# Optimization experiments

Hardware: AMD Instinct MI355X
Metric: run time of the kernel (lower is better)

Reference implementation:

```python
import jax, jax.numpy as jnp
import numpy as np

B, C, H, W = 2, 8, 256, 512


def _k3(x):
    """e_prod_KernelChannels3: 3x3 unroll -> [B,C,9,H,W].
    Channel k holds the neighbour at offset (k//3-1, k%3-1); middle (k=4) is ones
    ('e of middle = 1' per the docstring). ce arg of the torch module is unused."""
    b, c, h, w = x.shape
    p = jnp.pad(x, ((0, 0), (0, 0), (1, 1), (1, 1)))
    s = lambda dy, dx: p[:, :, dy:dy + h, dx:dx + w]
    return jnp.stack([s(0, 0), s(0, 1), s(0, 2),
                      s(1, 0), jnp.ones_like(x), s(1, 2),
                      s(2, 0), s(2, 1), s(2, 2)], axis=2)


def _forward(e, ce):
    b, c, h, w = e.shape
    e3 = _k3(e)    # kernel3(e, ce)
    ce3 = _k3(ce)  # kernel3(ce, e)
    e3p = jnp.pad(e3, ((0, 0), (0, 0), (0, 0), (1, 1), (1, 1)))
    ce3p = jnp.pad(ce3, ((0, 0), (0, 0), (0, 0), (1, 1), (1, 1)))
    E = lambda k: e3[:, :, k]
    Cc = lambda k: ce3[:, :, k]
    # torch pad-slices: ':-2'->start 0, '1:-1'->start 1, '2:'->start 2
    Ep = lambda k, r, cc: e3p[:, :, k, r:r + h, cc:cc + w]
    Cp = lambda k, r, cc: ce3p[:, :, k, r:r + h, cc:cc + w]

    def sel(ecands, ccands):
        es = jnp.stack(ecands, 0)          # [K,B,C,H,W]
        idx = jnp.argmax(jnp.stack(ccands, 0), axis=0)
        return jnp.take_along_axis(es, idx[None], axis=0)[0]

    e00 = E(0) * Ep(0, 0, 0)
    e04 = E(2) * Ep(2, 0, 2)
    e40 = E(6) * Ep(6, 2, 0)
    e44 = E(8) * Ep(8, 2, 2)
    e10 = sel([E(0) * Ep(3, 0, 0), E(3) * Ep(0, 1, 0)],
              [Cc(0) * Cp(3, 0, 0), Cc(3) * Cp(0, 1, 0)])
    e20 = sel([E(0) * Ep(6, 0, 0), E(3) * Ep(3, 1, 0), E(6) * Ep(0, 2, 0)],
              [Cc(0) * Cp(6, 0, 0), Cc(3) * Cp(3, 1, 0), Cc(6) * Cp(0, 2, 0)])
    e30 = sel([E(3) * Ep(6, 1, 0), E(6) * Ep(3, 2, 0)],
              [Cc(3) * Cp(6, 1, 0), Cc(6) * Cp(3, 2, 0)])
    e14 = sel([E(2) * Ep(5, 0, 2), E(5) * Ep(2, 1, 2)],
              [Cc(2) * Cp(5, 0, 2), Cc(5) * Cp(2, 1, 2)])
    # NOTE: source uses ce3_pad channel 3 (not 5) in the middle candidate -- kept faithfully
    e24 = sel([E(2) * Ep(8, 0, 2), E(5) * Ep(5, 1, 2), E(8) * Ep(2, 2, 2)],
              [Cc(2) * Cp(8, 0, 2), Cc(5) * Cp(3, 1, 2), Cc(8) * Cp(2, 2, 2)])
    e34 = sel([E(5) * Ep(8, 1, 2), E(8) * Ep(5, 2, 2)],
              [Cc(5) * Cp(8, 1, 2), Cc(8) * Cp(5, 2, 2)])
    e01 = sel([E(0) * Ep(1, 0, 0), E(1) * Ep(0, 0, 1)],
              [Cc(0) * Cp(1, 0, 0), Cc(1) * Cp(0, 0, 1)])
    e02 = sel([E(0) * Ep(2, 0, 0), E(1) * Ep(1, 0, 1), E(2) * Ep(0, 0, 2)],
              [Cc(0) * Cp(2, 0, 0), Cc(1) * Cp(1, 0, 1), Cc(2) * Cp(0, 0, 2)])
    e03 = sel([E(1) * Ep(2, 0, 1), E(2) * Ep(1, 0, 2)],
              [Cc(1) * Cp(2, 0, 1), Cc(2) * Cp(1, 0, 2)])
    e41 = sel([E(6) * Ep(7, 2, 0), E(7) * Ep(6, 2, 1)],
              [Cc(6) * Cp(7, 2, 0), Cc(7) * Cp(6, 2, 1)])
    e42 = sel([E(6) * Ep(8, 2, 0), E(7) * Ep(7, 2, 1), E(8) * Ep(6, 2, 2)],
              [Cc(6) * Cp(8, 2, 0), Cc(7) * Cp(7, 2, 1), Cc(8) * Cp(6, 2, 2)])
    e43 = sel([E(7) * Ep(8, 2, 1), E(8) * Ep(7, 2, 2)],
              [Cc(7) * Cp(8, 2, 1), Cc(8) * Cp(7, 2, 2)])
    return jnp.stack([e00, e01, e02, e03, e04,
                      e10, E(0), E(1), E(2), e14,
                      e20, E(3), E(4), E(5), e24,
                      e30, E(6), E(7), E(8), e34,
                      e40, e41, e42, e43, e44], axis=2)  # [B,C,25,H,W]


def setup_inputs() -> dict:
    key = jax.random.key(0)
    k1, k2 = jax.random.split(key)
    e = jax.random.uniform(k1, (B, C, H, W), dtype=jnp.float32)
    ce = jax.random.uniform(k2, (B, C, H, W), dtype=jnp.float32)
    return {"e": e, "ce": ce}


def reference(e, ce):
    return _forward(e, ce)
```

## Files before the change

### kernel.cpp

```cpp
#include <hip/hip_runtime.h>

#define BH 256
#define BW 512
#define BCN 16
#define HWSZ (BH * BW)

__global__ __launch_bounds__(256) void eprod25_kernel(
    const float* __restrict__ e, const float* __restrict__ ce,
    float* __restrict__ out)
{
    const int x  = blockIdx.x * 64 + (threadIdx.x & 63);
    const int y  = blockIdx.y * 4  + (threadIdx.x >> 6);
    const int bc = blockIdx.z;

    const float* __restrict__ ebase = e  + (size_t)bc * HWSZ;
    const float* __restrict__ cbase = ce + (size_t)bc * HWSZ;

    float ev[5][5], cv[5][5];
#pragma unroll
    for (int di = 0; di < 5; ++di) {
        const int iy = y - 2 + di;
        const bool rok = (unsigned)iy < (unsigned)BH;
#pragma unroll
        for (int dj = 0; dj < 5; ++dj) {
            const int ix = x - 2 + dj;
            const bool ok = rok && ((unsigned)ix < (unsigned)BW);
            const size_t idx = (size_t)iy * BW + ix;
            ev[di][dj] = ok ? ebase[idx] : 0.f;
            cv[di][dj] = ok ? cbase[idx] : 0.f;
        }
    }

    const float E0 = ev[1][1], E1 = ev[1][2], E2 = ev[1][3];
    const float E3 = ev[2][1],               E5 = ev[2][3];
    const float E6 = ev[3][1], E7 = ev[3][2], E8 = ev[3][3];
    const float C0 = cv[1][1], C1 = cv[1][2], C2 = cv[1][3];
    const float C3 = cv[2][1],               C5 = cv[2][3];
    const float C6 = cv[3][1], C7 = cv[3][2], C8 = cv[3][3];

    const bool rok0 = (y >= 1), rok2 = (y <= BH - 2);
    const bool cok0 = (x >= 1), cok2 = (x <= BW - 2);
    const bool m00 = rok0 && cok0, m01 = rok0, m02 = rok0 && cok2;
    const bool m10 = cok0,                     m12 = cok2;
    const bool m20 = rok2 && cok0, m21 = rok2, m22 = rok2 && cok2;

#define MV(arr, di, dj, m) ((m) ? arr[di][dj] : 0.f)

    auto sel2 = [](float a0, float a1, float c0, float c1) {
        return (c1 > c0) ? a1 : a0;
    };
    auto sel3 = [](float a0, float a1, float a2, float c0, float c1, float c2) {
        float best = c0, a = a0;
        if (c1 > best) { best = c1; a = a1; }
        if (c2 > best) { a = a2; }
        return a;
    };

    const float e00 = E0 * MV(ev, 0, 0, m00);
    const float e04 = E2 * MV(ev, 0, 4, m02);
    const float e40 = E6 * MV(ev, 4, 0, m20);
    const float e44 = E8 * MV(ev, 4, 4, m22);

    const float e10 = sel2(E0 * MV(ev, 1, 0, m00), E3 * MV(ev, 1, 0, m10),
                           C0 * MV(cv, 1, 0, m00), C3 * MV(cv, 1, 0, m10));
    const float e20 = sel3(E0 * MV(ev, 2, 0, m00), E3 * MV(ev, 2, 0, m10), E6 * MV(ev, 2, 0, m20),
                           C0 * MV(cv, 2, 0, m00), C3 * MV(cv, 2, 0, m10), C6 * MV(cv, 2, 0, m20));
    const float e30 = sel2(E3 * MV(ev, 3, 0, m10), E6 * MV(ev, 3, 0, m20),
                           C3 * MV(cv, 3, 0, m10), C6 * MV(cv, 3, 0, m20));

    const float e14 = sel2(E2 * MV(ev, 1, 4, m02), E5 * MV(ev, 1, 4, m12),
                           C2 * MV(cv, 1, 4, m02), C5 * MV(cv, 1, 4, m12));
    const float e24 = sel3(E2 * MV(ev, 2, 4, m02), E5 * MV(ev, 2, 4, m12), E8 * MV(ev, 2, 4, m22),
                           C2 * MV(cv, 2, 4, m02), C5 * MV(cv, 2, 2, m12), C8 * MV(cv, 2, 4, m22));
    const float e34 = sel2(E5 * MV(ev, 3, 4, m12), E8 * MV(ev, 3, 4, m22),
                           C5 * MV(cv, 3, 4, m12), C8 * MV(cv, 3, 4, m22));

    const float e01 = sel2(E0 * MV(ev, 0, 1, m00), E1 * MV(ev, 0, 1, m01),
                           C0 * MV(cv, 0, 1, m00), C1 * MV(cv, 0, 1, m01));
    const float e02 = sel3(E0 * MV(ev, 0, 2, m00), E1 * MV(ev, 0, 2, m01), E2 * MV(ev, 0, 2, m02),
                           C0 * MV(cv, 0, 2, m00), C1 * MV(cv, 0, 2, m01), C2 * MV(cv, 0, 2, m02));
    const float e03 = sel2(E1 * MV(ev, 0, 3, m01), E2 * MV(ev, 0, 3, m02),
                           C1 * MV(cv, 0, 3, m01), C2 * MV(cv, 0, 3, m02));

    const float e41 = sel2(E6 * MV(ev, 4, 1, m20), E7 * MV(ev, 4, 1, m21),
                           C6 * MV(cv, 4, 1, m20), C7 * MV(cv, 4, 1, m21));
    const float e42 = sel3(E6 * MV(ev, 4, 2, m20), E7 * MV(ev, 4, 2, m21), E8 * MV(ev, 4, 2, m22),
                           C6 * MV(cv, 4, 2, m20), C7 * MV(cv, 4, 2, m21), C8 * MV(cv, 4, 2, m22));
    const float e43 = sel2(E7 * MV(ev, 4, 3, m21), E8 * MV(ev, 4, 3, m22),
                           C7 * MV(cv, 4, 3, m21), C8 * MV(cv, 4, 3, m22));

#undef MV

    float o[25];
    o[0]  = e00; o[1]  = e01; o[2]  = e02; o[3]  = e03; o[4]  = e04;
    o[5]  = e10; o[6]  = E0;  o[7]  = E1;  o[8]  = E2;  o[9]  = e14;
    o[10] = e20; o[11] = E3;  o[12] = 1.f; o[13] = E5;  o[14] = e24;
    o[15] = e30; o[16] = E6;  o[17] = E7;  o[18] = E8;  o[19] = e34;
    o[20] = e40; o[21] = e41; o[22] = e42; o[23] = e43; o[24] = e44;

    float* __restrict__ obase = out + (size_t)bc * 25 * HWSZ + (size_t)y * BW + x;
#pragma unroll
    for (int k = 0; k < 25; ++k) {
        obase[(size_t)k * HWSZ] = o[k];
    }
}

extern "C" void kernel_launch(void* const* d_in, const int* in_sizes, int n_in,
                              void* d_out, int out_size, void* d_ws, size_t ws_size,
                              hipStream_t stream) {
    const float* e  = (const float*)d_in[0];
    const float* ce = (const float*)d_in[1];
    float* out = (float*)d_out;

    dim3 grid(BW / 64, BH / 4, BCN);
    dim3 block(256);
    eprod25_kernel<<<grid, block, 0, stream>>>(e, ce, out);
}
```

Baseline: 41.20 us.

## Process four pixels per thread with vectorized loads and nontemporal float4 stores

Each thread now computes four adjacent output pixels. It loads each stencil row as one float4 plus two float2 halo loads instead of 25 scalar loads per input, and writes each of the 25 output planes with a nontemporal float4 store. The grid shrinks fourfold in x. The goal is fewer memory instructions, reuse of overlapping neighbours between adjacent pixels, and less cache pollution from the large write-only output, at the cost of more registers per thread and fewer threads in flight.

```diff
diff --git a/kernel.cpp b/kernel.cpp
--- a/kernel.cpp
+++ b/kernel.cpp
@@ -5,46 +5,46 @@
 #define BCN 16
 #define HWSZ (BH * BW)
 
+typedef float f4 __attribute__((ext_vector_type(4)));
+typedef float f2 __attribute__((ext_vector_type(2)));
+
 __global__ __launch_bounds__(256) void eprod25_kernel(
     const float* __restrict__ e, const float* __restrict__ ce,
     float* __restrict__ out)
 {
-    const int x  = blockIdx.x * 64 + (threadIdx.x & 63);
-    const int y  = blockIdx.y * 4  + (threadIdx.x >> 6);
-    const int bc = blockIdx.z;
+    const int lane = threadIdx.x & 63;
+    const int wv   = threadIdx.x >> 6;
+    const int x4   = blockIdx.x * 256 + lane * 4;
+    const int y    = blockIdx.y * 4 + wv;
+    const int bc   = blockIdx.z;
 
     const float* __restrict__ ebase = e  + (size_t)bc * HWSZ;
     const float* __restrict__ cbase = ce + (size_t)bc * HWSZ;
 
-    float ev[5][5], cv[5][5];
+    float ev[5][8], cv[5][8];
+    const bool lok  = (x4 >= 2);
+    const bool rokx = (x4 <= BW - 6);
 #pragma unroll
     for (int di = 0; di < 5; ++di) {
         const int iy = y - 2 + di;
-        const bool rok = (unsigned)iy < (unsigned)BH;
-#pragma unroll
-        for (int dj = 0; dj < 5; ++dj) {
-            const int ix = x - 2 + dj;
-            const bool ok = rok && ((unsigned)ix < (unsigned)BW);
-            const size_t idx = (size_t)iy * BW + ix;
-            ev[di][dj] = ok ? ebase[idx] : 0.f;
-            cv[di][dj] = ok ? cbase[idx] : 0.f;
-        }
+        const bool rk = (unsigned)iy < (unsigned)BH;
+        const float* er = ebase + (size_t)iy * BW;
+        const float* cr = cbase + (size_t)iy * BW;
+        f4 ec = rk ? *(const f4*)(er + x4) : (f4)0.f;
+        f4 cc = rk ? *(const f4*)(cr + x4) : (f4)0.f;
+        f2 el = (rk && lok)  ? *(const f2*)(er + x4 - 2) : (f2)0.f;
+        f2 cl = (rk && lok)  ? *(const f2*)(cr + x4 - 2) : (f2)0.f;
+        f2 eg = (rk && rokx) ? *(const f2*)(er + x4 + 4) : (f2)0.f;
+        f2 cg = (rk && rokx) ? *(const f2*)(cr + x4 + 4) : (f2)0.f;
+        ev[di][0]=el[0]; ev[di][1]=el[1]; ev[di][2]=ec[0]; ev[di][3]=ec[1];
+        ev[di][4]=ec[2]; ev[di][5]=ec[3]; ev[di][6]=eg[0]; ev[di][7]=eg[1];
+        cv[di][0]=cl[0]; cv[di][1]=cl[1]; cv[di][2]=cc[0]; cv[di][3]=cc[1];
+        cv[di][4]=cc[2]; cv[di][5]=cc[3]; cv[di][6]=cg[0]; cv[di][7]=cg[1];
     }
 
-    const float E0 = ev[1][1], E1 = ev[1][2], E2 = ev[1][3];
-    const float E3 = ev[2][1],               E5 = ev[2][3];
-    const float E6 = ev[3][1], E7 = ev[3][2], E8 = ev[3][3];
-    const float C0 = cv[1][1], C1 = cv[1][2], C2 = cv[1][3];
-    const float C3 = cv[2][1],               C5 = cv[2][3];
-    const float C6 = cv[3][1], C7 = cv[3][2], C8 = cv[3][3];
+    const bool rok0 = (y >= 1), rok2 = (y <= BH - 2);
 
-    const bool rok0 = (y >= 1), rok2 = (y <= BH - 2);
-    const bool cok0 = (x >= 1), cok2 = (x <= BW - 2);
-    const bool m00 = rok0 && cok0, m01 = rok0, m02 = rok0 && cok2;
-    const bool m10 = cok0,                     m12 = cok2;
-    const bool m20 = rok2 && cok0, m21 = rok2, m22 = rok2 && cok2;
-
-#define MV(arr, di, dj, m) ((m) ? arr[di][dj] : 0.f)
+    float* __restrict__ obase = out + (size_t)bc * 25 * HWSZ + (size_t)y * BW + x4;
 
     auto sel2 = [](float a0, float a1, float c0, float c1) {
         return (c1 > c0) ? a1 : a0;
@@ -56,53 +56,71 @@
         return a;
     };
 
-    const float e00 = E0 * MV(ev, 0, 0, m00);
-    const float e04 = E2 * MV(ev, 0, 4, m02);
-    const float e40 = E6 * MV(ev, 4, 0, m20);
-    const float e44 = E8 * MV(ev, 4, 4, m22);
+    auto st4 = [&](int k, auto f) {
+        f4 v;
+        v[0] = f(0); v[1] = f(1); v[2] = f(2); v[3] = f(3);
+        __builtin_nontemporal_store(v, reinterpret_cast<f4*>(obase + (size_t)k * HWSZ));
+    };
 
-    const float e10 = sel2(E0 * MV(ev, 1, 0, m00), E3 * MV(ev, 1, 0, m10),
-                           C0 * MV(cv, 1, 0, m00), C3 * MV(cv, 1, 0, m10));
-    const float e20 = sel3(E0 * MV(ev, 2, 0, m00), E3 * MV(ev, 2, 0, m10), E6 * MV(ev, 2, 0, m20),
-                           C0 * MV(cv, 2, 0, m00), C3 * MV(cv, 2, 0, m10), C6 * MV(cv, 2, 0, m20));
-    const float e30 = sel2(E3 * MV(ev, 3, 0, m10), E6 * MV(ev, 3, 0, m20),
-                           C3 * MV(cv, 3, 0, m10), C6 * MV(cv, 3, 0, m20));
+#define PE(di, c) ev[di][p + (c)]
+#define PC(di, c) cv[di][p + (c)]
+#define MASKS \
+    const bool cok0 = (x4 + p >= 1); \
+    const bool cok2 = (x4 + p <= BW - 2); \
+    const bool m00 = rok0 && cok0; const bool m01 = rok0; const bool m02 = rok0 && cok2; \
+    const bool m10 = cok0; const bool m12 = cok2; \
+    const bool m20 = rok2 && cok0; const bool m21 = rok2; const bool m22 = rok2 && cok2; \
+    (void)m00; (void)m01; (void)m02; (void)m10; (void)m12; (void)m20; (void)m21; (void)m22;
+#define MVE(di, c, m) ((m) ? PE(di, c) : 0.f)
+#define MVC(di, c, m) ((m) ? PC(di, c) : 0.f)
 
-    const float e14 = sel2(E2 * MV(ev, 1, 4, m02), E5 * MV(ev, 1, 4, m12),
-                           C2 * MV(cv, 1, 4, m02), C5 * MV(cv, 1, 4, m12));
-    const float e24 = sel3(E2 * MV(ev, 2, 4, m02), E5 * MV(ev, 2, 4, m12), E8 * MV(ev, 2, 4, m22),
-                           C2 * MV(cv, 2, 4, m02), C5 * MV(cv, 2, 2, m12), C8 * MV(cv, 2, 4, m22));
-    const float e34 = sel2(E5 * MV(ev, 3, 4, m12), E8 * MV(ev, 3, 4, m22),
-                           C5 * MV(cv, 3, 4, m12), C8 * MV(cv, 3, 4, m22));
+    st4(0, [&](int p) { MASKS return PE(1,1) * MVE(0,0,m00); });
+    st4(1, [&](int p) { MASKS return sel2(PE(1,1)*MVE(0,1,m00), PE(1,2)*MVE(0,1,m01),
+                                          PC(1,1)*MVC(0,1,m00), PC(1,2)*MVC(0,1,m01)); });
+    st4(2, [&](int p) { MASKS return sel3(PE(1,1)*MVE(0,2,m00), PE(1,2)*MVE(0,2,m01), PE(1,3)*MVE(0,2,m02),
+                                          PC(1,1)*MVC(0,2,m00), PC(1,2)*MVC(0,2,m01), PC(1,3)*MVC(0,2,m02)); });
+    st4(3, [&](int p) { MASKS return sel2(PE(1,2)*MVE(0,3,m01), PE(1,3)*MVE(0,3,m02),
+                                          PC(1,2)*MVC(0,3,m01), PC(1,3)*MVC(0,3,m02)); });
+    st4(4, [&](int p) { MASKS return PE(1,3) * MVE(0,4,m02); });
 
-    const float e01 = sel2(E0 * MV(ev, 0, 1, m00), E1 * MV(ev, 0, 1, m01),
-                           C0 * MV(cv, 0, 1, m00), C1 * MV(cv, 0, 1, m01));
-    const float e02 = sel3(E0 * MV(ev, 0, 2, m00), E1 * MV(ev, 0, 2, m01), E2 * MV(ev, 0, 2, m02),
-                           C0 * MV(cv, 0, 2, m00), C1 * MV(cv, 0, 2, m01), C2 * MV(cv, 0, 2, m02));
-    const float e03 = sel2(E1 * MV(ev, 0, 3, m01), E2 * MV(ev, 0, 3, m02),
-                           C1 * MV(cv, 0, 3, m01), C2 * MV(cv, 0, 3, m02));
+    st4(5, [&](int p) { MASKS return sel2(PE(1,1)*MVE(1,0,m00), PE(2,1)*MVE(1,0,m10),
+                                          PC(1,1)*MVC(1,0,m00), PC(2,1)*MVC(1,0,m10)); });
+    st4(6, [&](int p) { return PE(1,1); });
+    st4(7, [&](int p) { return PE(1,2); });
+    st4(8, [&](int p) { return PE(1,3); });
+    st4(9, [&](int p) { MASKS return sel2(PE(1,3)*MVE(1,4,m02), PE(2,3)*MVE(1,4,m12),
+                                          PC(1,3)*MVC(1,4,m02), PC(2,3)*MVC(1,4,m12)); });
 
-    const float e41 = sel2(E6 * MV(ev, 4, 1, m20), E7 * MV(ev, 4, 1, m21),
-                           C6 * MV(cv, 4, 1, m20), C7 * MV(cv, 4, 1, m21));
-    const float e42 = sel3(E6 * MV(ev, 4, 2, m20), E7 * MV(ev, 4, 2, m21), E8 * MV(ev, 4, 2, m22),
-                           C6 * MV(cv, 4, 2, m20), C7 * MV(cv, 4, 2, m21), C8 * MV(cv, 4, 2, m22));
-    const float e43 = sel2(E7 * MV(ev, 4, 3, m21), E8 * MV(ev, 4, 3, m22),
-                           C7 * MV(cv, 4, 3, m21), C8 * MV(cv, 4, 3, m22));
+    st4(10, [&](int p) { MASKS return sel3(PE(1,1)*MVE(2,0,m00), PE(2,1)*MVE(2,0,m10), PE(3,1)*MVE(2,0,m20),
+                                           PC(1,1)*MVC(2,0,m00), PC(2,1)*MVC(2,0,m10), PC(3,1)*MVC(2,0,m20)); });
+    st4(11, [&](int p) { return PE(2,1); });
+    st4(12, [&](int p) { return 1.f; });
+    st4(13, [&](int p) { return PE(2,3); });
+    st4(14, [&](int p) { MASKS return sel3(PE(1,3)*MVE(2,4,m02), PE(2,3)*MVE(2,4,m12), PE(3,3)*MVE(2,4,m22),
+                                           PC(1,3)*MVC(2,4,m02), PC(2,3)*MVC(2,2,m12), PC(3,3)*MVC(2,4,m22)); });
 
-#undef MV
+    st4(15, [&](int p) { MASKS return sel2(PE(2,1)*MVE(3,0,m10), PE(3,1)*MVE(3,0,m20),
+                                           PC(2,1)*MVC(3,0,m10), PC(3,1)*MVC(3,0,m20)); });
+    st4(16, [&](int p) { return PE(3,1); });
+    st4(17, [&](int p) { return PE(3,2); });
+    st4(18, [&](int p) { return PE(3,3); });
+    st4(19, [&](int p) { MASKS return sel2(PE(2,3)*MVE(3,4,m12), PE(3,3)*MVE(3,4,m22),
+                                           PC(2,3)*MVC(3,4,m12), PC(3,3)*MVC(3,4,m22)); });
 
-    float o[25];
-    o[0]  = e00; o[1]  = e01; o[2]  = e02; o[3]  = e03; o[4]  = e04;
-    o[5]  = e10; o[6]  = E0;  o[7]  = E1;  o[8]  = E2;  o[9]  = e14;
-    o[10] = e20; o[11] = E3;  o[12] = 1.f; o[13] = E5;  o[14] = e24;
-    o[15] = e30; o[16] = E6;  o[17] = E7;  o[18] = E8;  o[19] = e34;
-    o[20] = e40; o[21] = e41; o[22] = e42; o[23] = e43; o[24] = e44;
+    st4(20, [&](int p) { MASKS return PE(3,1) * MVE(4,0,m20); });
+    st4(21, [&](int p) { MASKS return sel2(PE(3,1)*MVE(4,1,m20), PE(3,2)*MVE(4,1,m21),
+                                           PC(3,1)*MVC(4,1,m20), PC(3,2)*MVC(4,1,m21)); });
+    st4(22, [&](int p) { MASKS return sel3(PE(3,1)*MVE(4,2,m20), PE(3,2)*MVE(4,2,m21), PE(3,3)*MVE(4,2,m22),
+                                           PC(3,1)*MVC(4,2,m20), PC(3,2)*MVC(4,2,m21), PC(3,3)*MVC(4,2,m22)); });
+    st4(23, [&](int p) { MASKS return sel2(PE(3,2)*MVE(4,3,m21), PE(3,3)*MVE(4,3,m22),
+                                           PC(3,2)*MVC(4,3,m21), PC(3,3)*MVC(4,3,m22)); });
+    st4(24, [&](int p) { MASKS return PE(3,3) * MVE(4,4,m22); });
 
-    float* __restrict__ obase = out + (size_t)bc * 25 * HWSZ + (size_t)y * BW + x;
-#pragma unroll
-    for (int k = 0; k < 25; ++k) {
-        obase[(size_t)k * HWSZ] = o[k];
-    }
+#undef PE
+#undef PC
+#undef MASKS
+#undef MVE
+#undef MVC
 }
 
 extern "C" void kernel_launch(void* const* d_in, const int* in_sizes, int n_in,
@@ -112,7 +130,7 @@
     const float* ce = (const float*)d_in[1];
     float* out = (float*)d_out;
 
-    dim3 grid(BW / 64, BH / 4, BCN);
+    dim3 grid(BW / 256, BH / 4, BCN);
     dim3 block(256);
     eprod25_kernel<<<grid, block, 0, stream>>>(e, ce, out);
 }
```

New measurement: 41.35 us. No clear change (+0.4%).
